# Kernel tuning notes

Hardware: AMD Instinct MI355X
Metric: run time of the kernel (lower is better)

## Reference

```python
import jax, jax.numpy as jnp
import numpy as np

NODES = 23   # 22 players + ball per frame-graph
K = 8        # random neighbors per node
B, T = 64, 128
G = B * T            # total graphs (frames)
N = G * NODES        # total nodes
D_IN, H, RH = 16, 128, 128


def setup_inputs() -> dict:
    key = jax.random.key(0)
    ks = jax.random.split(key, 10)
    x = jax.random.normal(ks[0], (N, D_IN), jnp.float32)
    # per-graph random edges: dst = each node repeated K times, src = random node in same graph
    src_local = jax.random.randint(ks[1], (G, NODES * K), 0, NODES)
    dst_local = jnp.tile(jnp.repeat(jnp.arange(NODES), K)[None, :], (G, 1))
    off = (jnp.arange(G) * NODES)[:, None]
    edge_index = jnp.stack([(src_local + off).reshape(-1),
                            (dst_local + off).reshape(-1)]).astype(jnp.int32)
    runner_idx = jax.random.randint(ks[2], (G,), 0, NODES, dtype=jnp.int32)
    sc = lambda k, sh: (jax.random.normal(k, sh, jnp.float32) * 0.05)
    return {
        'x': x, 'edge_index': edge_index, 'runner_idx': runner_idx,
        'W1': sc(ks[3], (D_IN, H)), 'b1': jnp.zeros((H,), jnp.float32),
        'W2': sc(ks[4], (H, H)),    'b2': jnp.zeros((H,), jnp.float32),
        'W_ih': sc(ks[5], (3 * RH, H)), 'W_hh': sc(ks[6], (3 * RH, RH)),
        'b_ih': jnp.zeros((3 * RH,), jnp.float32), 'b_hh': jnp.zeros((3 * RH,), jnp.float32),
        'Wp': sc(ks[7], (RH, 2)), 'bp': jnp.zeros((2,), jnp.float32),
    }


def _gcn_conv(h, edge_index, W, b):
    # PyG GCNConv: add self-loops, symmetric normalization, scatter-sum
    h = h @ W
    loop = jnp.arange(N, dtype=edge_index.dtype)
    s = jnp.concatenate([edge_index[0], loop])
    d = jnp.concatenate([edge_index[1], loop])
    deg = jax.ops.segment_sum(jnp.ones_like(s, h.dtype), d, num_segments=N)
    dinv = jnp.where(deg > 0, jax.lax.rsqrt(deg), 0.0)
    norm = dinv[s] * dinv[d]                      # [E+N]
    out = jax.ops.segment_sum(h[s] * norm[:, None], d, num_segments=N)
    return out + b


def _gru(seq, W_ih, W_hh, b_ih, b_hh):
    # torch GRU: gates in r,z,n order
    xg = seq @ W_ih.T + b_ih                      # [B,T,3RH]
    def step(hprev, xt):
        gh = hprev @ W_hh.T + b_hh
        xr, xz, xn = jnp.split(xt, 3, axis=-1)
        hr, hz, hn = jnp.split(gh, 3, axis=-1)
        r = jax.nn.sigmoid(xr + hr)
        z = jax.nn.sigmoid(xz + hz)
        n = jnp.tanh(xn + r * hn)
        hnew = (1.0 - z) * n + z * hprev
        return hnew, hnew
    h0 = jnp.zeros((seq.shape[0], RH), seq.dtype)
    _, outs = jax.lax.scan(step, h0, jnp.swapaxes(xg, 0, 1))
    return jnp.swapaxes(outs, 0, 1)               # [B,T,RH]


def reference(x, edge_index, runner_idx, W1, b1, W2, b2,
              W_ih, W_hh, b_ih, b_hh, Wp, bp):
    h = jax.nn.relu(_gcn_conv(x, edge_index, W1, b1))
    h = jax.nn.relu(_gcn_conv(h, edge_index, W2, b2))
    # fused equivalent of the per-graph nonzero()/indexing loop:
    runner_global = jnp.arange(G, dtype=jnp.int32) * NODES + runner_idx
    seq = h[runner_global].reshape(B, T, H)       # all lengths == T, padding is a no-op
    out = _gru(seq, W_ih, W_hh, b_ih, b_hh)
    return out @ Wp + bp                          # [B,T,2]
```

## Files before the change

### kernel.cpp

```cpp
#include <hip/hip_runtime.h>
#include <hip/hip_bf16.h>
#include <math.h>

#define GG 8192
#define NODESN 23
#define KK 8
#define DIN 16
#define HH 128
#define RHH 128
#define EPG (NODESN*KK)
#define TTT 128
#define BBB 64

template<int CTRL>
static __device__ __forceinline__ float dpp_add(float v) {
    int x = __builtin_amdgcn_update_dpp(0, __float_as_int(v), CTRL, 0xF, 0xF, true);
    return v + __int_as_float(x);
}
#define DPP_XOR1 0xB1
#define DPP_XOR2 0x4E
#define DPP_SHL4 0x104

__global__ __launch_bounds__(256) void gcn_hsum(
    const float* __restrict__ x, const int* __restrict__ esrc,
    const int* __restrict__ runner,
    const float* __restrict__ W1, const float* __restrict__ b1,
    float* __restrict__ hsum_g)
{
    __shared__ float xs[NODESN * DIN];
    __shared__ int   srcs[EPG];
    __shared__ float t1[NODESN * HH];
    __shared__ float red[256];

    const int g   = blockIdx.x;
    const int tid = threadIdx.x;
    const int j   = tid & 127;
    const int nh  = tid >> 7;

    for (int i = tid; i < NODESN * DIN; i += 256) xs[i] = x[g * NODESN * DIN + i];
    for (int i = tid; i < EPG; i += 256)          srcs[i] = esrc[g * EPG + i] - g * NODESN;

    float w[DIN];
    #pragma unroll
    for (int k = 0; k < DIN; k++) w[k] = W1[k * HH + j];
    const float b1j = b1[j];
    __syncthreads();

    const int n0 = nh * 12;
    const int n1 = nh ? NODESN : 12;
    for (int n = n0; n < n1; n++) {
        float acc = 0.f;
        #pragma unroll
        for (int k = 0; k < DIN; k += 4) {
            float4 xv = *(const float4*)&xs[n * DIN + k];
            acc = fmaf(xv.x, w[k], fmaf(xv.y, w[k+1], fmaf(xv.z, w[k+2], fmaf(xv.w, w[k+3], acc))));
        }
        t1[n * HH + j] = acc;
    }
    __syncthreads();

    const int r = runner[g];
    float part = 0.f;
    for (int slot = nh; slot < 9; slot += 2) {
        int node = (slot < 8) ? srcs[r * KK + slot] : r;
        float acc = t1[node * HH + j];
        #pragma unroll
        for (int k = 0; k < KK; k++) acc += t1[srcs[node * KK + k] * HH + j];
        part += fmaxf(acc * (1.f / 9.f) + b1j, 0.f);
    }
    red[tid] = part;
    __syncthreads();
    if (tid < HH) hsum_g[(size_t)g * HH + tid] = red[tid] + red[tid + 128];
}

__global__ __launch_bounds__(256) void seq_kernel(
    const float* __restrict__ hsum_g, const float* __restrict__ W2,
    const float* __restrict__ b2, float* __restrict__ seq)
{
    __shared__ float hs[16 * HH];
    const int tid = threadIdx.x;
    const int j = tid & 127, mh = tid >> 7;
    const size_t base = (size_t)blockIdx.x * 16 * HH;

    for (int v = tid; v < 16 * HH / 4; v += 256)
        ((float4*)hs)[v] = ((const float4*)(hsum_g + base))[v];
    __syncthreads();

    float acc[8];
    #pragma unroll
    for (int m = 0; m < 8; m++) acc[m] = 0.f;
    const float* hrow = hs + mh * 8 * HH;
    for (int k = 0; k < HH; k += 4) {
        float w0  = W2[(k+0)*HH + j];
        float w1  = W2[(k+1)*HH + j];
        float w2v = W2[(k+2)*HH + j];
        float w3  = W2[(k+3)*HH + j];
        #pragma unroll
        for (int m = 0; m < 8; m++) {
            float4 hv = *(const float4*)&hrow[m * HH + k];
            acc[m] = fmaf(hv.x, w0, fmaf(hv.y, w1, fmaf(hv.z, w2v, fmaf(hv.w, w3, acc[m]))));
        }
    }
    const float bj = b2[j];
    #pragma unroll
    for (int m = 0; m < 8; m++)
        seq[base + (size_t)(mh * 8 + m) * HH + j] = fmaxf(acc[m] * (1.f/9.f) + bj, 0.f);
}

__global__ void transpose_wih(const float* __restrict__ W, float* __restrict__ WT)
{
    int idx = blockIdx.x * 256 + threadIdx.x;
    if (idx < 3 * RHH * RHH) {
        int jj = idx / RHH, kk = idx - jj * RHH;
        WT[kk * (3 * RHH) + jj] = W[idx];
    }
}

__global__ __launch_bounds__(384) void xg_kernel(
    const float* __restrict__ seq, const float* __restrict__ WT,
    const float* __restrict__ b_ih, float* __restrict__ xg)
{
    const int tid = threadIdx.x;
    const int m0 = blockIdx.x * 8;
    const float* srow = seq + (size_t)m0 * RHH;
    float acc[8];
    const float bv = b_ih[tid];
    #pragma unroll
    for (int mi = 0; mi < 8; mi++) acc[mi] = bv;
    for (int k = 0; k < RHH; k += 4) {
        float w0 = WT[(k+0)*384 + tid];
        float w1 = WT[(k+1)*384 + tid];
        float w2 = WT[(k+2)*384 + tid];
        float w3 = WT[(k+3)*384 + tid];
        #pragma unroll
        for (int mi = 0; mi < 8; mi++) {
            float4 sv = *(const float4*)(srow + mi * RHH + k);
            acc[mi] = fmaf(sv.x, w0, fmaf(sv.y, w1, fmaf(sv.z, w2, fmaf(sv.w, w3, acc[mi]))));
        }
    }
    #pragma unroll
    for (int mi = 0; mi < 8; mi++)
        xg[(size_t)(m0 + mi) * 384 + tid] = acc[mi];
}

#define CHUNK 32
#define XGB_FLOATS (CHUNK * HH * 4)

__global__ __launch_bounds__(512)
__attribute__((amdgpu_waves_per_eu(2, 2)))
void gru_kernel(
    const float* __restrict__ xg, const float* __restrict__ W_hh,
    const float* __restrict__ b_hh, const float* __restrict__ Wp,
    const float* __restrict__ bp, float* __restrict__ out)
{
    __shared__ float xgbuf[XGB_FLOATS];
    __shared__ float houtb[(CHUNK + 2) * HH];
    __shared__ float wps[2 * RHH + 2];

    const int b   = blockIdx.x;
    const int tid = threadIdx.x;
    const int q   = tid & 3;
    const int i   = tid >> 2;

    float4 wrv[8], wzv[8], wnv[8];
    int lof[8];
    {
        const float* br = W_hh + (size_t)i * RHH + q * 32;
        const float* bz = br + (size_t)RHH * RHH;
        const float* bn = bz + (size_t)RHH * RHH;
        #pragma unroll
        for (int m = 0; m < 8; m++) {
            int p = (m + 2 * q) & 7;
            lof[m] = q * 32 + 4 * p;
            wrv[m] = *(const float4*)(br + 4 * p);
            wzv[m] = *(const float4*)(bz + 4 * p);
            wnv[m] = *(const float4*)(bn + 4 * p);
        }
    }
    const float bhr = b_hh[i];
    const float bhz = b_hh[RHH + i];
    const float bhn = b_hh[2 * RHH + i];

    if (tid < 2 * RHH) wps[tid] = Wp[tid];
    if (tid < 2)       wps[2 * RHH + tid] = bp[tid];
    if (tid < HH)      houtb[CHUNK * HH + tid] = 0.f;
    float hprev = 0.f;

    const float* xbase = xg + (size_t)b * TTT * 3 * RHH;
    float* outb = out + (size_t)b * TTT * 2;

    for (int c = 0; c < TTT / CHUNK; c++) {
        #pragma unroll
        for (int k2 = 0; k2 < 8; k2++) {
            int slot = tid + (k2 << 9);
            int tl = slot >> 7, ii = slot & 127;
            const float* gsrc = xbase + (size_t)(c * CHUNK + tl) * 384 + ii;
            float4 v;
            v.x = gsrc[0]; v.y = gsrc[128]; v.z = gsrc[256]; v.w = 0.f;
            *(float4*)&xgbuf[slot << 2] = v;
        }
        if (c > 0) {
            const int s  = tid & 7;
            const int cc = (tid >> 3) & 1;
            const int tl = tid >> 4;
            const float* hr = &houtb[(tl + 1) * HH + s * 16];
            float acc = 0.f;
            #pragma unroll
            for (int m = 0; m < 16; m += 4) {
                float4 hv = *(const float4*)(hr + m);
                int k = s * 16 + m;
                acc = fmaf(hv.x, wps[(k+0)*2 + cc],
                      fmaf(hv.y, wps[(k+1)*2 + cc],
                      fmaf(hv.z, wps[(k+2)*2 + cc],
                      fmaf(hv.w, wps[(k+3)*2 + cc], acc))));
            }
            acc = dpp_add<DPP_XOR1>(acc);
            acc = dpp_add<DPP_XOR2>(acc);
            acc = dpp_add<DPP_SHL4>(acc);
            if (s == 0)
                outb[((c - 1) * CHUNK + tl) * 2 + cc] = acc + wps[2 * RHH + cc];
        }
        __syncthreads();

        for (int tl = 0; tl < CHUNK; tl++) {
            const float* hrow = &houtb[(tl == 0 ? CHUNK : tl) * HH];
            float4 xgv = *(const float4*)&xgbuf[(tl * HH + i) << 2];
            float ar = 0.f, az = 0.f, an = 0.f;
            #pragma unroll
            for (int m = 0; m < 8; m++) {
                float4 hv = *(const float4*)(hrow + lof[m]);
                ar = fmaf(hv.x, wrv[m].x, fmaf(hv.y, wrv[m].y, fmaf(hv.z, wrv[m].z, fmaf(hv.w, wrv[m].w, ar))));
                az = fmaf(hv.x, wzv[m].x, fmaf(hv.y, wzv[m].y, fmaf(hv.z, wzv[m].z, fmaf(hv.w, wzv[m].w, az))));
                an = fmaf(hv.x, wnv[m].x, fmaf(hv.y, wnv[m].y, fmaf(hv.z, wnv[m].z, fmaf(hv.w, wnv[m].w, an))));
            }
            ar = dpp_add<DPP_XOR1>(ar); ar = dpp_add<DPP_XOR2>(ar);
            az = dpp_add<DPP_XOR1>(az); az = dpp_add<DPP_XOR2>(az);
            an = dpp_add<DPP_XOR1>(an); an = dpp_add<DPP_XOR2>(an);

            float sr = xgv.x + ar + bhr;
            float sz = xgv.y + az + bhz;
            float rg = 1.f / (1.f + __expf(-sr));
            float zg = 1.f / (1.f + __expf(-sz));
            float tv = fmaf(rg, an + bhn, xgv.z);
            tv = fminf(fmaxf(tv, -15.f), 15.f);
            float e2 = __expf(-2.f * tv);
            float ng = (1.f - e2) / (1.f + e2);
            hprev = fmaf(zg, hprev, (1.f - zg) * ng);
            if (q == 0) houtb[(tl + 1) * HH + i] = hprev;
            __syncthreads();
        }
    }

    {
        const int s  = tid & 7;
        const int cc = (tid >> 3) & 1;
        const int tl = tid >> 4;
        const float* hr = &houtb[(tl + 1) * HH + s * 16];
        float acc = 0.f;
        #pragma unroll
        for (int m = 0; m < 16; m += 4) {
            float4 hv = *(const float4*)(hr + m);
            int k = s * 16 + m;
            acc = fmaf(hv.x, wps[(k+0)*2 + cc],
                  fmaf(hv.y, wps[(k+1)*2 + cc],
                  fmaf(hv.z, wps[(k+2)*2 + cc],
                  fmaf(hv.w, wps[(k+3)*2 + cc], acc))));
        }
        acc = dpp_add<DPP_XOR1>(acc);
        acc = dpp_add<DPP_XOR2>(acc);
        acc = dpp_add<DPP_SHL4>(acc);
        if (s == 0)
            outb[((TTT / CHUNK - 1) * CHUNK + tl) * 2 + cc] = acc + wps[2 * RHH + cc];
    }
}

extern "C" void kernel_launch(void* const* d_in, const int* in_sizes, int n_in,
                              void* d_out, int out_size, void* d_ws, size_t ws_size,
                              hipStream_t stream)
{
    const float* x      = (const float*)d_in[0];
    const int*   eidx   = (const int*)d_in[1];
    const int*   runner = (const int*)d_in[2];
    const float* W1     = (const float*)d_in[3];
    const float* b1     = (const float*)d_in[4];
    const float* W2     = (const float*)d_in[5];
    const float* b2     = (const float*)d_in[6];
    const float* W_ih   = (const float*)d_in[7];
    const float* W_hh   = (const float*)d_in[8];
    const float* b_ih   = (const float*)d_in[9];
    const float* b_hh   = (const float*)d_in[10];
    const float* Wp     = (const float*)d_in[11];
    const float* bp     = (const float*)d_in[12];
    float* out = (float*)d_out;

    float* seq    = (float*)d_ws;
    float* xg     = seq + (size_t)GG * HH;
    float* WT     = xg + (size_t)GG * 3 * RHH;
    float* hsum_g = xg;

    transpose_wih<<<192, 256, 0, stream>>>(W_ih, WT);
    gcn_hsum<<<GG, 256, 0, stream>>>(x, eidx, runner, W1, b1, hsum_g);
    seq_kernel<<<GG / 16, 256, 0, stream>>>(hsum_g, W2, b2, seq);
    xg_kernel<<<GG / 8, 384, 0, stream>>>(seq, WT, b_ih, xg);
    gru_kernel<<<BBB, 512, 0, stream>>>(xg, W_hh, b_hh, Wp, bp, out);
}
```

Before: 243.3 us.

## Halve GRU block to 256 threads, each computing two hidden units per step

```diff
diff --git a/kernel.cpp b/kernel.cpp
--- a/kernel.cpp
+++ b/kernel.cpp
@@ -19,7 +19,6 @@
 }
 #define DPP_XOR1 0xB1
 #define DPP_XOR2 0x4E
-#define DPP_SHL4 0x104
 
 __global__ __launch_bounds__(256) void gcn_hsum(
     const float* __restrict__ x, const int* __restrict__ esrc,
@@ -144,55 +143,64 @@
 }
 
 #define CHUNK 32
+#define HPAD 132
 #define XGB_FLOATS (CHUNK * HH * 4)
 
-__global__ __launch_bounds__(512)
-__attribute__((amdgpu_waves_per_eu(2, 2)))
+__global__ __launch_bounds__(256)
+__attribute__((amdgpu_waves_per_eu(1, 1)))
 void gru_kernel(
     const float* __restrict__ xg, const float* __restrict__ W_hh,
     const float* __restrict__ b_hh, const float* __restrict__ Wp,
     const float* __restrict__ bp, float* __restrict__ out)
 {
     __shared__ float xgbuf[XGB_FLOATS];
-    __shared__ float houtb[(CHUNK + 2) * HH];
+    __shared__ float houtb[(CHUNK + 2) * HPAD];
     __shared__ float wps[2 * RHH + 2];
 
     const int b   = blockIdx.x;
     const int tid = threadIdx.x;
     const int q   = tid & 3;
-    const int i   = tid >> 2;
-
-    float4 wrv[8], wzv[8], wnv[8];
+    const int g   = tid >> 2;
+
+    const int i0 = g, i1 = g + 64;
+
+    float4 wr0[8], wz0[8], wn0[8], wr1[8], wz1[8], wn1[8];
     int lof[8];
     {
-        const float* br = W_hh + (size_t)i * RHH + q * 32;
-        const float* bz = br + (size_t)RHH * RHH;
-        const float* bn = bz + (size_t)RHH * RHH;
+        const float* r0 = W_hh + (size_t)i0 * RHH;
+        const float* z0 = r0 + (size_t)RHH * RHH;
+        const float* n0 = z0 + (size_t)RHH * RHH;
+        const float* r1 = W_hh + (size_t)i1 * RHH;
+        const float* z1 = r1 + (size_t)RHH * RHH;
+        const float* n1 = z1 + (size_t)RHH * RHH;
         #pragma unroll
         for (int m = 0; m < 8; m++) {
             int p = (m + 2 * q) & 7;
-            lof[m] = q * 32 + 4 * p;
-            wrv[m] = *(const float4*)(br + 4 * p);
-            wzv[m] = *(const float4*)(bz + 4 * p);
-            wnv[m] = *(const float4*)(bn + 4 * p);
-        }
-    }
-    const float bhr = b_hh[i];
-    const float bhz = b_hh[RHH + i];
-    const float bhn = b_hh[2 * RHH + i];
+            int o = q * 32 + 4 * p;
+            lof[m] = o;
+            wr0[m] = *(const float4*)(r0 + o);
+            wz0[m] = *(const float4*)(z0 + o);
+            wn0[m] = *(const float4*)(n0 + o);
+            wr1[m] = *(const float4*)(r1 + o);
+            wz1[m] = *(const float4*)(z1 + o);
+            wn1[m] = *(const float4*)(n1 + o);
+        }
+    }
+    const float bhr0 = b_hh[i0], bhz0 = b_hh[RHH + i0], bhn0 = b_hh[2 * RHH + i0];
+    const float bhr1 = b_hh[i1], bhz1 = b_hh[RHH + i1], bhn1 = b_hh[2 * RHH + i1];
 
     if (tid < 2 * RHH) wps[tid] = Wp[tid];
     if (tid < 2)       wps[2 * RHH + tid] = bp[tid];
-    if (tid < HH)      houtb[CHUNK * HH + tid] = 0.f;
-    float hprev = 0.f;
+    if (tid < HH)      houtb[CHUNK * HPAD + tid] = 0.f;
+    float hp0 = 0.f, hp1 = 0.f;
 
     const float* xbase = xg + (size_t)b * TTT * 3 * RHH;
     float* outb = out + (size_t)b * TTT * 2;
 
     for (int c = 0; c < TTT / CHUNK; c++) {
-        #pragma unroll
-        for (int k2 = 0; k2 < 8; k2++) {
-            int slot = tid + (k2 << 9);
+        #pragma unroll 4
+        for (int k2 = 0; k2 < 16; k2++) {
+            int slot = tid + (k2 << 8);
             int tl = slot >> 7, ii = slot & 127;
             const float* gsrc = xbase + (size_t)(c * CHUNK + tl) * 384 + ii;
             float4 v;
@@ -200,15 +208,15 @@
             *(float4*)&xgbuf[slot << 2] = v;
         }
         if (c > 0) {
-            const int s  = tid & 7;
-            const int cc = (tid >> 3) & 1;
-            const int tl = tid >> 4;
-            const float* hr = &houtb[(tl + 1) * HH + s * 16];
+            const int s  = tid & 3;
+            const int cc = (tid >> 2) & 1;
+            const int tl = tid >> 3;
+            const float* hr = &houtb[(tl + 1) * HPAD + s * 32];
             float acc = 0.f;
             #pragma unroll
-            for (int m = 0; m < 16; m += 4) {
+            for (int m = 0; m < 32; m += 4) {
                 float4 hv = *(const float4*)(hr + m);
-                int k = s * 16 + m;
+                int k = s * 32 + m;
                 acc = fmaf(hv.x, wps[(k+0)*2 + cc],
                       fmaf(hv.y, wps[(k+1)*2 + cc],
                       fmaf(hv.z, wps[(k+2)*2 + cc],
@@ -216,51 +224,73 @@
             }
             acc = dpp_add<DPP_XOR1>(acc);
             acc = dpp_add<DPP_XOR2>(acc);
-            acc = dpp_add<DPP_SHL4>(acc);
             if (s == 0)
                 outb[((c - 1) * CHUNK + tl) * 2 + cc] = acc + wps[2 * RHH + cc];
         }
         __syncthreads();
 
         for (int tl = 0; tl < CHUNK; tl++) {
-            const float* hrow = &houtb[(tl == 0 ? CHUNK : tl) * HH];
-            float4 xgv = *(const float4*)&xgbuf[(tl * HH + i) << 2];
-            float ar = 0.f, az = 0.f, an = 0.f;
+            const float* hrow = &houtb[(tl == 0 ? CHUNK : tl) * HPAD];
+            float4 x0 = *(const float4*)&xgbuf[(tl * HH + i0) << 2];
+            float4 x1 = *(const float4*)&xgbuf[(tl * HH + i1) << 2];
+            float ar0 = 0.f, az0 = 0.f, an0 = 0.f, ar1 = 0.f, az1 = 0.f, an1 = 0.f;
             #pragma unroll
             for (int m = 0; m < 8; m++) {
                 float4 hv = *(const float4*)(hrow + lof[m]);
-                ar = fmaf(hv.x, wrv[m].x, fmaf(hv.y, wrv[m].y, fmaf(hv.z, wrv[m].z, fmaf(hv.w, wrv[m].w, ar))));
-                az = fmaf(hv.x, wzv[m].x, fmaf(hv.y, wzv[m].y, fmaf(hv.z, wzv[m].z, fmaf(hv.w, wzv[m].w, az))));
-                an = fmaf(hv.x, wnv[m].x, fmaf(hv.y, wnv[m].y, fmaf(hv.z, wnv[m].z, fmaf(hv.w, wnv[m].w, an))));
-            }
-            ar = dpp_add<DPP_XOR1>(ar); ar = dpp_add<DPP_XOR2>(ar);
-            az = dpp_add<DPP_XOR1>(az); az = dpp_add<DPP_XOR2>(az);
-            an = dpp_add<DPP_XOR1>(an); an = dpp_add<DPP_XOR2>(an);
-
-            float sr = xgv.x + ar + bhr;
-            float sz = xgv.y + az + bhz;
-            float rg = 1.f / (1.f + __expf(-sr));
-            float zg = 1.f / (1.f + __expf(-sz));
-            float tv = fmaf(rg, an + bhn, xgv.z);
-            tv = fminf(fmaxf(tv, -15.f), 15.f);
-            float e2 = __expf(-2.f * tv);
-            float ng = (1.f - e2) / (1.f + e2);
-            hprev = fmaf(zg, hprev, (1.f - zg) * ng);
-            if (q == 0) houtb[(tl + 1) * HH + i] = hprev;
+                ar0 = fmaf(hv.x, wr0[m].x, fmaf(hv.y, wr0[m].y, fmaf(hv.z, wr0[m].z, fmaf(hv.w, wr0[m].w, ar0))));
+                az0 = fmaf(hv.x, wz0[m].x, fmaf(hv.y, wz0[m].y, fmaf(hv.z, wz0[m].z, fmaf(hv.w, wz0[m].w, az0))));
+                an0 = fmaf(hv.x, wn0[m].x, fmaf(hv.y, wn0[m].y, fmaf(hv.z, wn0[m].z, fmaf(hv.w, wn0[m].w, an0))));
+                ar1 = fmaf(hv.x, wr1[m].x, fmaf(hv.y, wr1[m].y, fmaf(hv.z, wr1[m].z, fmaf(hv.w, wr1[m].w, ar1))));
+                az1 = fmaf(hv.x, wz1[m].x, fmaf(hv.y, wz1[m].y, fmaf(hv.z, wz1[m].z, fmaf(hv.w, wz1[m].w, az1))));
+                an1 = fmaf(hv.x, wn1[m].x, fmaf(hv.y, wn1[m].y, fmaf(hv.z, wn1[m].z, fmaf(hv.w, wn1[m].w, an1))));
+            }
+            ar0 = dpp_add<DPP_XOR1>(ar0); ar0 = dpp_add<DPP_XOR2>(ar0);
+            az0 = dpp_add<DPP_XOR1>(az0); az0 = dpp_add<DPP_XOR2>(az0);
+            an0 = dpp_add<DPP_XOR1>(an0); an0 = dpp_add<DPP_XOR2>(an0);
+            ar1 = dpp_add<DPP_XOR1>(ar1); ar1 = dpp_add<DPP_XOR2>(ar1);
+            az1 = dpp_add<DPP_XOR1>(az1); az1 = dpp_add<DPP_XOR2>(az1);
+            an1 = dpp_add<DPP_XOR1>(an1); an1 = dpp_add<DPP_XOR2>(an1);
+
+            {
+                float sr = x0.x + ar0 + bhr0;
+                float sz = x0.y + az0 + bhz0;
+                float rg = 1.f / (1.f + __expf(-sr));
+                float zg = 1.f / (1.f + __expf(-sz));
+                float tv = fmaf(rg, an0 + bhn0, x0.z);
+                tv = fminf(fmaxf(tv, -15.f), 15.f);
+                float e2 = __expf(-2.f * tv);
+                float ng = (1.f - e2) / (1.f + e2);
+                hp0 = fmaf(zg, hp0, (1.f - zg) * ng);
+            }
+            {
+                float sr = x1.x + ar1 + bhr1;
+                float sz = x1.y + az1 + bhz1;
+                float rg = 1.f / (1.f + __expf(-sr));
+                float zg = 1.f / (1.f + __expf(-sz));
+                float tv = fmaf(rg, an1 + bhn1, x1.z);
+                tv = fminf(fmaxf(tv, -15.f), 15.f);
+                float e2 = __expf(-2.f * tv);
+                float ng = (1.f - e2) / (1.f + e2);
+                hp1 = fmaf(zg, hp1, (1.f - zg) * ng);
+            }
+            if (q == 0) {
+                houtb[(tl + 1) * HPAD + i0] = hp0;
+                houtb[(tl + 1) * HPAD + i1] = hp1;
+            }
             __syncthreads();
         }
     }
 
     {
-        const int s  = tid & 7;
-        const int cc = (tid >> 3) & 1;
-        const int tl = tid >> 4;
-        const float* hr = &houtb[(tl + 1) * HH + s * 16];
+        const int s  = tid & 3;
+        const int cc = (tid >> 2) & 1;
+        const int tl = tid >> 3;
+        const float* hr = &houtb[(tl + 1) * HPAD + s * 32];
         float acc = 0.f;
         #pragma unroll
-        for (int m = 0; m < 16; m += 4) {
+        for (int m = 0; m < 32; m += 4) {
             float4 hv = *(const float4*)(hr + m);
-            int k = s * 16 + m;
+            int k = s * 32 + m;
             acc = fmaf(hv.x, wps[(k+0)*2 + cc],
                   fmaf(hv.y, wps[(k+1)*2 + cc],
                   fmaf(hv.z, wps[(k+2)*2 + cc],
@@ -268,7 +298,6 @@
         }
         acc = dpp_add<DPP_XOR1>(acc);
         acc = dpp_add<DPP_XOR2>(acc);
-        acc = dpp_add<DPP_SHL4>(acc);
         if (s == 0)
             outb[((TTT / CHUNK - 1) * CHUNK + tl) * 2 + cc] = acc + wps[2 * RHH + cc];
     }
@@ -302,5 +331,5 @@
     gcn_hsum<<<GG, 256, 0, stream>>>(x, eidx, runner, W1, b1, hsum_g);
     seq_kernel<<<GG / 16, 256, 0, stream>>>(hsum_g, W2, b2, seq);
     xg_kernel<<<GG / 8, 384, 0, stream>>>(seq, WT, b_ih, xg);
-    gru_kernel<<<BBB, 512, 0, stream>>>(xg, W_hh, b_hh, Wp, bp, out);
-}
+    gru_kernel<<<BBB, 256, 0, stream>>>(xg, W_hh, b_hh, Wp, bp, out);
+}
```

After: 308.1 us. 1.27x slower.
